# Optimization experiments

Hardware: AMD Instinct MI355X
Metric: run time of the kernel (lower is better)

Reference implementation:

```python
import jax, jax.numpy as jnp
import numpy as np

B, F, V, E = 4096, 26, 20000, 64
LAYERS = [256, 128, 1]


def setup_inputs() -> dict:
    key = jax.random.key(0)
    ks = jax.random.split(key, 13)
    s = 1.0 / np.sqrt(E)
    inp = {
        "x_idx": jax.random.randint(ks[0], (B, F), 0, V),
        # per-field embedding tables [F, V, E] and linear (bias) tables [F, V, 1]
        "embed_w": jax.random.normal(ks[1], (F, V, E), jnp.float32) * 0.01,
        "embed_b": jax.random.normal(ks[2], (F, V, 1), jnp.float32) * 0.01,
        "attention_w": jax.random.normal(ks[3], (E, E), jnp.float32) * s,
        "attention_b": jax.random.normal(ks[4], (1, E), jnp.float32) * 0.01,
        "attention_p": jax.random.normal(ks[5], (E,), jnp.float32) * 0.01,
        "w0": jax.random.normal(ks[6], (E, LAYERS[0]), jnp.float32) * s,
        "b0": jnp.zeros((LAYERS[0],), jnp.float32),
        "w1": jax.random.normal(ks[7], (LAYERS[0], LAYERS[1]), jnp.float32) * (1.0 / np.sqrt(LAYERS[0])),
        "b1": jnp.zeros((LAYERS[1],), jnp.float32),
        "w2": jax.random.normal(ks[8], (LAYERS[1], LAYERS[2]), jnp.float32) * (1.0 / np.sqrt(LAYERS[1])),
        "b2": jnp.zeros((LAYERS[2],), jnp.float32),
        "bias": jnp.zeros((1,), jnp.float32),
    }
    return inp


def _gather_fields(tables, idx):
    # tables: [F, V, D], idx: [B, F] -> [B, F, D]
    return jax.vmap(lambda tbl, i: tbl[i], in_axes=(0, 1), out_axes=1)(tables, idx)


def reference(x_idx, embed_w, embed_b, attention_w, attention_b, attention_p,
              w0, b0, w1, b1, w2, b2, bias):
    f = embed_w.shape[0]
    xw = _gather_fields(embed_w, x_idx)                      # [B, F, E]
    iu, ju = jnp.triu_indices(f, k=1)                        # P = F*(F-1)/2 pairs, loop order i<j
    pairs = xw[:, iu, :] * xw[:, ju, :]                      # [B, P, E] pairwise FM interactions
    # attention network: relu(pairs @ W + b), score = <p, .>, softmax over pairs
    att_h = jax.nn.relu(jnp.einsum('bpe,ef->bpf', pairs, attention_w) + attention_b)
    scores = jnp.sum(attention_p * att_h, axis=2, keepdims=True)   # [B, P, 1]
    att_out = jax.nn.softmax(scores, axis=1)                       # softmax pooling over pairs
    afm = jnp.sum(att_out * pairs, axis=1)                         # [B, E]
    # MLP head
    h = jax.nn.relu(afm @ w0 + b0)
    h = jax.nn.relu(h @ w1 + b1)
    bilinear = h @ w2 + b2                                         # [B, 1]
    # linear (LR) term from per-field bias tables
    lr = jnp.sum(_gather_fields(embed_b, x_idx), axis=1)           # [B, 1]
    return bilinear + lr + bias
```

## Files before the change

### kernel.cpp

```cpp
#include <hip/hip_runtime.h>
#include <stdint.h>

#define B_N 4096
#define F_N 26
#define V_N 20000
#define E_N 64
#define P_N 325
#define PT  21
#define SPB 8

typedef __attribute__((ext_vector_type(8))) _Float16 half8;
typedef __attribute__((ext_vector_type(4))) _Float16 half4;
typedef __attribute__((ext_vector_type(4))) float floatx4;

__global__ __launch_bounds__(512, 2) void anfm_attn_kernel(
    const int* __restrict__ x_idx, const float* __restrict__ embed_w,
    const float* __restrict__ embed_b, const float* __restrict__ att_w,
    const float* __restrict__ att_b, const float* __restrict__ att_p,
    float* __restrict__ ws_afm, float* __restrict__ ws_lr)
{
    __shared__ _Float16 xwb[SPB][F_N][72];
    __shared__ _Float16 WT[64][72];
    __shared__ unsigned short pijL[336];
    __shared__ float apL[64], abL[64];

    const int tid  = threadIdx.x;
    const int lane = tid & 63;
    const int wid  = tid >> 6;
    const int c16  = lane & 15;
    const int g    = lane >> 4;
    const int b    = blockIdx.x * SPB + wid;

    int myidx = (lane < F_N) ? x_idx[b * F_N + lane] : 0;
    float lv  = (lane < F_N) ? embed_b[lane * V_N + myidx] : 0.f;
    float4 gv[7];
    #pragma unroll
    for (int it = 0; it < 7; it++) {
        int f = it * 4 + g;
        int fc = (f < F_N) ? f : 0;
        int idxf = __shfl(myidx, fc);
        const float4* src = reinterpret_cast<const float4*>(
            embed_w + ((size_t)(fc * V_N + idxf)) * E_N);
        gv[it] = src[c16];
    }

    if (tid < 336) {
        int p = tid;
        int i = 0, j = 1;
        if (p < P_N) {
            i = (int)((51.0f - sqrtf(2601.0f - 8.0f * (float)p)) * 0.5f);
            if (i * (51 - i) / 2 > p) i--;
            else if ((i + 1) * (50 - i) / 2 <= p) i++;
            j = p - i * (51 - i) / 2 + i + 1;
        }
        pijL[p] = (unsigned short)((i << 8) | j);
    } else if (tid < 400) {
        apL[tid - 336] = att_p[tid - 336];
    } else if (tid < 464) {
        abL[tid - 400] = att_b[tid - 400];
    }
    for (int idx = tid; idx < 64 * 64; idx += 512) {
        int k = idx >> 6, col = idx & 63;
        WT[col][k] = (_Float16)att_w[idx];
    }

    #pragma unroll
    for (int it = 0; it < 7; it++) {
        int f = it * 4 + g;
        if (f < F_N) {
            float4 v = gv[it];
            half4 hv = {(_Float16)v.x, (_Float16)v.y, (_Float16)v.z, (_Float16)v.w};
            *reinterpret_cast<half4*>(&xwb[wid][f][c16 * 4]) = hv;
        }
    }
    __syncthreads();

    half8 bfr[4][2];
    #pragma unroll
    for (int nt = 0; nt < 4; nt++)
        #pragma unroll
        for (int s = 0; s < 2; s++)
            bfr[nt][s] = *reinterpret_cast<const half8*>(
                &WT[nt * 16 + c16][s * 32 + g * 8]);

    float acf[16];
    #pragma unroll
    for (int u = 0; u < 16; u++) acf[u] = 0.f;
    float Zp = 0.f;

    #pragma unroll 1
    for (int t = 0; t < PT; t++) {
        int pk = pijL[t * 16 + c16];
        int ri = pk >> 8, rj = pk & 255;
        half8 af[2];
        #pragma unroll
        for (int s = 0; s < 2; s++) {
            half8 xv = *reinterpret_cast<const half8*>(&xwb[wid][ri][s * 32 + g * 8]);
            half8 yv = *reinterpret_cast<const half8*>(&xwb[wid][rj][s * 32 + g * 8]);
            af[s] = xv * yv;
        }
        float scq = 0.f;
        #pragma unroll
        for (int nt = 0; nt < 4; nt++) {
            floatx4 acc = *reinterpret_cast<const floatx4*>(&abL[nt * 16 + g * 4]);
            acc = __builtin_amdgcn_mfma_f32_16x16x32_f16(bfr[nt][0], af[0], acc, 0, 0, 0);
            acc = __builtin_amdgcn_mfma_f32_16x16x32_f16(bfr[nt][1], af[1], acc, 0, 0, 0);
            floatx4 ap4 = *reinterpret_cast<const floatx4*>(&apL[nt * 16 + g * 4]);
            #pragma unroll
            for (int r = 0; r < 4; r++)
                scq = fmaf(ap4[r], fmaxf(acc[r], 0.f), scq);
        }
        scq += __shfl_xor(scq, 16);
        scq += __shfl_xor(scq, 32);
        float w = (t * 16 + c16 < P_N) ? __expf(scq) : 0.f;
        Zp += w;
        #pragma unroll
        for (int s = 0; s < 2; s++)
            #pragma unroll
            for (int u = 0; u < 8; u++)
                acf[s * 8 + u] = fmaf((float)af[s][u], w, acf[s * 8 + u]);
    }

    #pragma unroll
    for (int msk = 1; msk <= 8; msk <<= 1) {
        Zp += __shfl_xor(Zp, msk);
        #pragma unroll
        for (int u = 0; u < 16; u++) acf[u] += __shfl_xor(acf[u], msk);
    }

    if (c16 == 0) {
        float rZ = 1.f / Zp;
        #pragma unroll
        for (int s = 0; s < 2; s++) {
            floatx4 o0 = {acf[s * 8 + 0] * rZ, acf[s * 8 + 1] * rZ,
                          acf[s * 8 + 2] * rZ, acf[s * 8 + 3] * rZ};
            floatx4 o1 = {acf[s * 8 + 4] * rZ, acf[s * 8 + 5] * rZ,
                          acf[s * 8 + 6] * rZ, acf[s * 8 + 7] * rZ};
            *reinterpret_cast<floatx4*>(&ws_afm[(size_t)b * 64 + s * 32 + g * 8])     = o0;
            *reinterpret_cast<floatx4*>(&ws_afm[(size_t)b * 64 + s * 32 + g * 8 + 4]) = o1;
        }
    }
    #pragma unroll
    for (int off = 32; off; off >>= 1) lv += __shfl_xor(lv, off);
    if (lane == 0) ws_lr[b] = lv;
}

__global__ __launch_bounds__(256, 4) void anfm_mlp_kernel(
    const float* __restrict__ ws_afm, const float* __restrict__ ws_lr,
    const float* __restrict__ w0, const float* __restrict__ b0,
    const float* __restrict__ w1, const float* __restrict__ b1,
    const float* __restrict__ w2, const float* __restrict__ b2,
    const float* __restrict__ bias, float* __restrict__ out)
{
    __shared__ _Float16 afmL[16][72];
    __shared__ _Float16 h0L[16][264];
    __shared__ float    h1L[16][132];

    const int tid  = threadIdx.x;
    const int lane = tid & 63;
    const int wid  = tid >> 6;
    const int c16  = lane & 15;
    const int g    = lane >> 4;
    const int blk  = blockIdx.x;

    for (int it = tid; it < 16 * 64; it += 256) {
        int s = it >> 6, e = it & 63;
        afmL[s][e] = (_Float16)ws_afm[((size_t)blk * 16 + s) * 64 + e];
    }
    __syncthreads();

    {
        half8 af[2];
        #pragma unroll
        for (int s = 0; s < 2; s++)
            af[s] = *reinterpret_cast<const half8*>(&afmL[c16][s * 32 + g * 8]);
        #pragma unroll
        for (int q = 0; q < 4; q++) {
            int n = (wid * 4 + q) * 16 + c16;
            half8 bf[2];
            #pragma unroll
            for (int s = 0; s < 2; s++)
                #pragma unroll
                for (int u = 0; u < 8; u++)
                    bf[s][u] = (_Float16)w0[(s * 32 + g * 8 + u) * 256 + n];
            floatx4 acc = {0.f, 0.f, 0.f, 0.f};
            acc = __builtin_amdgcn_mfma_f32_16x16x32_f16(af[0], bf[0], acc, 0, 0, 0);
            acc = __builtin_amdgcn_mfma_f32_16x16x32_f16(af[1], bf[1], acc, 0, 0, 0);
            float b0n = b0[n];
            #pragma unroll
            for (int r = 0; r < 4; r++)
                h0L[g * 4 + r][n] = (_Float16)fmaxf(acc[r] + b0n, 0.f);
        }
    }
    __syncthreads();

    #pragma unroll
    for (int q = 0; q < 2; q++) {
        int n = (wid * 2 + q) * 16 + c16;
        floatx4 acc = {0.f, 0.f, 0.f, 0.f};
        #pragma unroll
        for (int ks = 0; ks < 8; ks++) {
            half8 af = *reinterpret_cast<const half8*>(&h0L[c16][ks * 32 + g * 8]);
            half8 bf;
            #pragma unroll
            for (int u = 0; u < 8; u++)
                bf[u] = (_Float16)w1[(ks * 32 + g * 8 + u) * 128 + n];
            acc = __builtin_amdgcn_mfma_f32_16x16x32_f16(af, bf, acc, 0, 0, 0);
        }
        float b1n = b1[n];
        #pragma unroll
        for (int r = 0; r < 4; r++)
            h1L[g * 4 + r][n] = fmaxf(acc[r] + b1n, 0.f);
    }
    __syncthreads();

    float w2a = w2[lane * 2], w2b = w2[lane * 2 + 1];
    float base = b2[0] + bias[0];
    #pragma unroll
    for (int s = 0; s < 4; s++) {
        int m = wid * 4 + s;
        float part = fmaf(h1L[m][lane * 2], w2a, h1L[m][lane * 2 + 1] * w2b);
        #pragma unroll
        for (int off = 32; off; off >>= 1) part += __shfl_xor(part, off);
        if (lane == 0) {
            int sg = blk * 16 + m;
            out[sg] = part + base + ws_lr[sg];
        }
    }
}

extern "C" void kernel_launch(void* const* d_in, const int* in_sizes, int n_in,
                              void* d_out, int out_size, void* d_ws, size_t ws_size,
                              hipStream_t stream) {
    const int*   x_idx   = (const int*)d_in[0];
    const float* embed_w = (const float*)d_in[1];
    const float* embed_b = (const float*)d_in[2];
    const float* att_w   = (const float*)d_in[3];
    const float* att_b   = (const float*)d_in[4];
    const float* att_p   = (const float*)d_in[5];
    const float* w0      = (const float*)d_in[6];
    const float* b0      = (const float*)d_in[7];
    const float* w1      = (const float*)d_in[8];
    const float* b1      = (const float*)d_in[9];
    const float* w2      = (const float*)d_in[10];
    const float* b2      = (const float*)d_in[11];
    const float* bias    = (const float*)d_in[12];

    float* ws_afm = (float*)d_ws;
    float* ws_lr  = ws_afm + (size_t)B_N * E_N;
    float* out    = (float*)d_out;

    anfm_attn_kernel<<<B_N / SPB, 512, 0, stream>>>(x_idx, embed_w, embed_b,
                                                    att_w, att_b, att_p,
                                                    ws_afm, ws_lr);
    anfm_mlp_kernel<<<B_N / 16, 256, 0, stream>>>(ws_afm, ws_lr,
                                                  w0, b0, w1, b1, w2, b2, bias, out);
}
```

Measured before the change: 42.20 us.

## Fuse attention pooling and MLP head into a single kernel

Merges the attention kernel and the MLP kernel into one launch. The pooled AFM vector and the LR term now stay in shared memory as fp16 and floats instead of going through the global workspace. The 8 samples of a block are padded to a 16-row MFMA tile with zeros, and the MLP work is redistributed across 8 waves. Launch bounds rise to 4 blocks per CU. This removes the second launch and the workspace round trip, but half of each MLP MFMA tile is wasted on padding rows, MLP weights are reloaded by twice as many blocks, and the higher occupancy target may cause register spills.

```diff
diff --git a/kernel.cpp b/kernel.cpp
--- a/kernel.cpp
+++ b/kernel.cpp
@@ -13,16 +13,23 @@
 typedef __attribute__((ext_vector_type(4))) _Float16 half4;
 typedef __attribute__((ext_vector_type(4))) float floatx4;
 
-__global__ __launch_bounds__(512, 2) void anfm_attn_kernel(
+__global__ __launch_bounds__(512, 4) void anfm_fused_kernel(
     const int* __restrict__ x_idx, const float* __restrict__ embed_w,
     const float* __restrict__ embed_b, const float* __restrict__ att_w,
     const float* __restrict__ att_b, const float* __restrict__ att_p,
-    float* __restrict__ ws_afm, float* __restrict__ ws_lr)
+    const float* __restrict__ w0, const float* __restrict__ b0,
+    const float* __restrict__ w1, const float* __restrict__ b1,
+    const float* __restrict__ w2, const float* __restrict__ b2,
+    const float* __restrict__ bias, float* __restrict__ out)
 {
     __shared__ _Float16 xwb[SPB][F_N][72];
     __shared__ _Float16 WT[64][72];
     __shared__ unsigned short pijL[336];
     __shared__ float apL[64], abL[64];
+    __shared__ _Float16 afmL[16][72];
+    __shared__ _Float16 h0L[16][264];
+    __shared__ float    h1L[16][132];
+    __shared__ float    lrL[SPB];
 
     const int tid  = threadIdx.x;
     const int lane = tid & 63;
@@ -59,6 +66,10 @@
     } else if (tid < 464) {
         abL[tid - 400] = att_b[tid - 400];
     }
+    for (int z = tid; z < 576; z += 512) {
+        int r = z / 72, c = z - r * 72;
+        afmL[8 + r][c] = (_Float16)0.f;
+    }
     for (int idx = tid; idx < 64 * 64; idx += 512) {
         int k = idx >> 6, col = idx & 63;
         WT[col][k] = (_Float16)att_w[idx];
@@ -132,51 +143,28 @@
         float rZ = 1.f / Zp;
         #pragma unroll
         for (int s = 0; s < 2; s++) {
-            floatx4 o0 = {acf[s * 8 + 0] * rZ, acf[s * 8 + 1] * rZ,
-                          acf[s * 8 + 2] * rZ, acf[s * 8 + 3] * rZ};
-            floatx4 o1 = {acf[s * 8 + 4] * rZ, acf[s * 8 + 5] * rZ,
-                          acf[s * 8 + 6] * rZ, acf[s * 8 + 7] * rZ};
-            *reinterpret_cast<floatx4*>(&ws_afm[(size_t)b * 64 + s * 32 + g * 8])     = o0;
-            *reinterpret_cast<floatx4*>(&ws_afm[(size_t)b * 64 + s * 32 + g * 8 + 4]) = o1;
+            half4 o0 = {(_Float16)(acf[s * 8 + 0] * rZ), (_Float16)(acf[s * 8 + 1] * rZ),
+                        (_Float16)(acf[s * 8 + 2] * rZ), (_Float16)(acf[s * 8 + 3] * rZ)};
+            half4 o1 = {(_Float16)(acf[s * 8 + 4] * rZ), (_Float16)(acf[s * 8 + 5] * rZ),
+                        (_Float16)(acf[s * 8 + 6] * rZ), (_Float16)(acf[s * 8 + 7] * rZ)};
+            *reinterpret_cast<half4*>(&afmL[wid][s * 32 + g * 8])     = o0;
+            *reinterpret_cast<half4*>(&afmL[wid][s * 32 + g * 8 + 4]) = o1;
         }
     }
     #pragma unroll
     for (int off = 32; off; off >>= 1) lv += __shfl_xor(lv, off);
-    if (lane == 0) ws_lr[b] = lv;
-}
-
-__global__ __launch_bounds__(256, 4) void anfm_mlp_kernel(
-    const float* __restrict__ ws_afm, const float* __restrict__ ws_lr,
-    const float* __restrict__ w0, const float* __restrict__ b0,
-    const float* __restrict__ w1, const float* __restrict__ b1,
-    const float* __restrict__ w2, const float* __restrict__ b2,
-    const float* __restrict__ bias, float* __restrict__ out)
-{
-    __shared__ _Float16 afmL[16][72];
-    __shared__ _Float16 h0L[16][264];
-    __shared__ float    h1L[16][132];
-
-    const int tid  = threadIdx.x;
-    const int lane = tid & 63;
-    const int wid  = tid >> 6;
-    const int c16  = lane & 15;
-    const int g    = lane >> 4;
-    const int blk  = blockIdx.x;
-
-    for (int it = tid; it < 16 * 64; it += 256) {
-        int s = it >> 6, e = it & 63;
-        afmL[s][e] = (_Float16)ws_afm[((size_t)blk * 16 + s) * 64 + e];
-    }
-    __syncthreads();
+    if (lane == 0) lrL[wid] = lv;
+    __syncthreads();
+
 
     {
-        half8 af[2];
+        half8 af0[2];
         #pragma unroll
         for (int s = 0; s < 2; s++)
-            af[s] = *reinterpret_cast<const half8*>(&afmL[c16][s * 32 + g * 8]);
-        #pragma unroll
-        for (int q = 0; q < 4; q++) {
-            int n = (wid * 4 + q) * 16 + c16;
+            af0[s] = *reinterpret_cast<const half8*>(&afmL[c16][s * 32 + g * 8]);
+        #pragma unroll
+        for (int q = 0; q < 2; q++) {
+            int n = (wid * 2 + q) * 16 + c16;
             half8 bf[2];
             #pragma unroll
             for (int s = 0; s < 2; s++)
@@ -184,8 +172,8 @@
                 for (int u = 0; u < 8; u++)
                     bf[s][u] = (_Float16)w0[(s * 32 + g * 8 + u) * 256 + n];
             floatx4 acc = {0.f, 0.f, 0.f, 0.f};
-            acc = __builtin_amdgcn_mfma_f32_16x16x32_f16(af[0], bf[0], acc, 0, 0, 0);
-            acc = __builtin_amdgcn_mfma_f32_16x16x32_f16(af[1], bf[1], acc, 0, 0, 0);
+            acc = __builtin_amdgcn_mfma_f32_16x16x32_f16(af0[0], bf[0], acc, 0, 0, 0);
+            acc = __builtin_amdgcn_mfma_f32_16x16x32_f16(af0[1], bf[1], acc, 0, 0, 0);
             float b0n = b0[n];
             #pragma unroll
             for (int r = 0; r < 4; r++)
@@ -194,18 +182,17 @@
     }
     __syncthreads();
 
-    #pragma unroll
-    for (int q = 0; q < 2; q++) {
-        int n = (wid * 2 + q) * 16 + c16;
+    {
+        int n = wid * 16 + c16;
         floatx4 acc = {0.f, 0.f, 0.f, 0.f};
         #pragma unroll
         for (int ks = 0; ks < 8; ks++) {
-            half8 af = *reinterpret_cast<const half8*>(&h0L[c16][ks * 32 + g * 8]);
+            half8 af1 = *reinterpret_cast<const half8*>(&h0L[c16][ks * 32 + g * 8]);
             half8 bf;
             #pragma unroll
             for (int u = 0; u < 8; u++)
                 bf[u] = (_Float16)w1[(ks * 32 + g * 8 + u) * 128 + n];
-            acc = __builtin_amdgcn_mfma_f32_16x16x32_f16(af, bf, acc, 0, 0, 0);
+            acc = __builtin_amdgcn_mfma_f32_16x16x32_f16(af1, bf, acc, 0, 0, 0);
         }
         float b1n = b1[n];
         #pragma unroll
@@ -214,18 +201,13 @@
     }
     __syncthreads();
 
-    float w2a = w2[lane * 2], w2b = w2[lane * 2 + 1];
-    float base = b2[0] + bias[0];
-    #pragma unroll
-    for (int s = 0; s < 4; s++) {
-        int m = wid * 4 + s;
-        float part = fmaf(h1L[m][lane * 2], w2a, h1L[m][lane * 2 + 1] * w2b);
+    {
+        float part = fmaf(h1L[wid][lane * 2], w2[lane * 2],
+                          h1L[wid][lane * 2 + 1] * w2[lane * 2 + 1]);
         #pragma unroll
         for (int off = 32; off; off >>= 1) part += __shfl_xor(part, off);
-        if (lane == 0) {
-            int sg = blk * 16 + m;
-            out[sg] = part + base + ws_lr[sg];
-        }
+        if (lane == 0)
+            out[blockIdx.x * SPB + wid] = part + b2[0] + bias[0] + lrL[wid];
     }
 }
 
@@ -245,14 +227,9 @@
     const float* w2      = (const float*)d_in[10];
     const float* b2      = (const float*)d_in[11];
     const float* bias    = (const float*)d_in[12];
-
-    float* ws_afm = (float*)d_ws;
-    float* ws_lr  = ws_afm + (size_t)B_N * E_N;
-    float* out    = (float*)d_out;
-
-    anfm_attn_kernel<<<B_N / SPB, 512, 0, stream>>>(x_idx, embed_w, embed_b,
-                                                    att_w, att_b, att_p,
-                                                    ws_afm, ws_lr);
-    anfm_mlp_kernel<<<B_N / 16, 256, 0, stream>>>(ws_afm, ws_lr,
-                                                  w0, b0, w1, b1, w2, b2, bias, out);
+    float*       out     = (float*)d_out;
+
+    anfm_fused_kernel<<<B_N / SPB, 512, 0, stream>>>(
+        x_idx, embed_w, embed_b, att_w, att_b, att_p,
+        w0, b0, w1, b1, w2, b2, bias, out);
 }
```

Result: faster. 34.28 us (-18.8%).
